# Kernel tuning notes

Measured on AMD Instinct MI355X. Metric: run time of the kernel, lower is better.

The kernel has to match this reference:

```python
import jax, jax.numpy as jnp
import numpy as np

B = 32          # patients
D = 128         # hidden dim (modality_embedding_dim == total_hidden_dim)
H = 4           # attention heads
DH = D // H     # per-head dim
L = 2           # num_graph_layers
N = {'ct': 1024, 'pet': 1024, 'clin': 256, 'gen': 2048, 'pat': 1}
# (src_type, dst_type) for the 8 relation types registered in _setup_relations
REL = [('ct','ct'), ('pet','pet'), ('clin','clin'), ('gen','gen'),
       ('pat','clin'), ('ct','gen'), ('pet','gen'), ('gen','pat')]
E_REL = [8192, 8192, 2048, 16384, 256, 8192, 8192, 2048]
EDGE_NAMES = ['e_ct','e_pet','e_clin','e_gen','e_pat2clin','e_ct2gen','e_pet2gen','e_gen2pat']


def setup_inputs() -> dict:
    key = jax.random.key(0)
    ks = iter(jax.random.split(key, 64))
    nk = lambda: next(ks)
    inp = {}
    inp['x_ct']   = jax.random.normal(nk(), (B, N['ct'],  D), jnp.float32)
    inp['x_pet']  = jax.random.normal(nk(), (B, N['pet'], D), jnp.float32)
    inp['x_clin'] = jax.random.normal(nk(), (B, N['clin'],D), jnp.float32)
    inp['x_gen']  = jax.random.normal(nk(), (B, N['gen'], D), jnp.float32)
    inp['early']  = jax.random.normal(nk(), (B, D), jnp.float32)

    def mk_edges(k, E, ns, nd):
        k1, k2 = jax.random.split(k)
        src = jax.random.randint(k1, (B, 1, E), 0, ns, jnp.int32)
        dst = jax.random.randint(k2, (B, 1, E), 0, nd, jnp.int32)
        return jnp.concatenate([src, dst], axis=1)  # [B,2,E]

    for nm, (s, d), E in zip(EDGE_NAMES, REL, E_REL):
        inp[nm] = mk_edges(nk(), E, N[s], N[d])

    sw = 1.0 / np.sqrt(D)
    inp['W_src'] = jax.random.normal(nk(), (L, 8, D, D), jnp.float32) * sw
    inp['W_dst'] = jax.random.normal(nk(), (L, 8, D, D), jnp.float32) * sw
    inp['a_src'] = jax.random.normal(nk(), (L, 8, H, DH), jnp.float32) * sw
    inp['a_dst'] = jax.random.normal(nk(), (L, 8, H, DH), jnp.float32) * sw
    inp['Wp'] = jax.random.normal(nk(), (3, D, D), jnp.float32) * sw  # CT, PET, genomic pooling
    inp['bp'] = jnp.zeros((3, D), jnp.float32)
    inp['W_sem'] = jax.random.normal(nk(), (4 * D, 128), jnp.float32) * (1.0 / np.sqrt(4 * D))
    inp['b_sem'] = jnp.zeros((128,), jnp.float32)
    inp['q_sem'] = jax.random.normal(nk(), (128,), jnp.float32) * sw
    return inp


def _leaky_relu(x):
    return jnp.where(x > 0, x, 0.2 * x)


def _gat_layer(x, edges, Ws, Wd, As, Ad):
    """One heterogeneous multi-head GAT layer summing over relation types."""
    agg = {t: jnp.zeros((B, N[t], H, DH), jnp.float32) for t in N}
    for r, ((s, d), ei) in enumerate(zip(REL, edges)):
        hs = jnp.einsum('bnd,de->bne', x[s], Ws[r]).reshape(B, N[s], H, DH)
        hd = jnp.einsum('bnd,de->bne', x[d], Wd[r]).reshape(B, N[d], H, DH)
        al_s = jnp.sum(hs * As[r], axis=-1)  # [B,Ns,H]
        al_d = jnp.sum(hd * Ad[r], axis=-1)  # [B,Nd,H]
        nd = N[d]

        def one(hs_b, as_b, ad_b, e_b):
            src, dst = e_b[0], e_b[1]
            logit = _leaky_relu(as_b[src] + ad_b[dst])                      # [E,H]
            m = jnp.full((nd, H), -1e30, logit.dtype).at[dst].max(logit)    # segment max
            p = jnp.exp(logit - m[dst])
            den = jnp.zeros((nd, H), p.dtype).at[dst].add(p)
            w = p / (den[dst] + 1e-16)                                      # edge softmax per dst node
            msg = w[:, :, None] * hs_b[src]                                 # [E,H,DH]
            return jnp.zeros((nd, H, DH), msg.dtype).at[dst].add(msg)

        agg[d] = agg[d] + jax.vmap(one)(hs, al_s, al_d, ei)
    return {t: jax.nn.elu(agg[t].reshape(B, N[t], D)) for t in N}


def _pool(feat, W, b):
    # query = Linear(mean(features)); scores = feat @ q; softmax-weighted sum
    q = jnp.mean(feat, axis=1) @ W + b            # [B,D]
    sc = jnp.einsum('bnd,bd->bn', feat, q)        # [B,N]
    w = jax.nn.softmax(sc, axis=1)
    return jnp.einsum('bn,bnd->bd', w, feat)      # [B,D]


def _forward(x_ct, x_pet, x_clin, x_gen, early, edges,
             W_src, W_dst, a_src, a_dst, Wp, bp, W_sem, b_sem, q_sem):
    x = {'ct': x_ct, 'pet': x_pet, 'clin': x_clin, 'gen': x_gen,
         'pat': early[:, None, :]}
    for l in range(L):
        x = _gat_layer(x, edges, W_src[l], W_dst[l], a_src[l], a_dst[l])
    ct_p  = _pool(x['ct'],  Wp[0], bp[0])
    pet_p = _pool(x['pet'], Wp[1], bp[1])
    gen_p = _pool(x['gen'], Wp[2], bp[2])   # shared across the 3 meta-paths
    pad = jnp.zeros((B, 2 * D), ct_p.dtype)  # pad 2D -> 4D as in original
    imm = jnp.concatenate([ct_p, gen_p, pad], axis=1)
    pro = jnp.concatenate([pet_p, gen_p, pad], axis=1)
    trt = jnp.concatenate([(ct_p + pet_p) * 0.5, gen_p, pad], axis=1)
    z = jnp.stack([imm, pro, trt], axis=1)                     # [B,3,4D]
    s = jnp.einsum('bpa,a->bp', jnp.tanh(jnp.einsum('bpf,fa->bpa', z, W_sem) + b_sem), q_sem)
    beta = jax.nn.softmax(s, axis=1)                           # [B,3]
    fused = jnp.einsum('bp,bpf->bf', beta, z)                  # [B,4D]
    return fused, beta


def reference(x_ct, x_pet, x_clin, x_gen, early,
              e_ct, e_pet, e_clin, e_gen, e_pat2clin, e_ct2gen, e_pet2gen, e_gen2pat,
              W_src, W_dst, a_src, a_dst, Wp, bp, W_sem, b_sem, q_sem):
    edges = [e_ct, e_pet, e_clin, e_gen, e_pat2clin, e_ct2gen, e_pet2gen, e_gen2pat]
    return _forward(x_ct, x_pet, x_clin, x_gen, early, edges,
                    W_src, W_dst, a_src, a_dst, Wp, bp, W_sem, b_sem, q_sem)
```

## Files before the change

kernel.cpp:

```cpp
#include <hip/hip_runtime.h>
#include <math.h>

static constexpr int NB = 32;
static constexpr int ND = 128;

typedef short bf16x8 __attribute__((ext_vector_type(8)));
typedef float f32x4  __attribute__((ext_vector_type(4)));
typedef unsigned short u16x8 __attribute__((ext_vector_type(8)));

__device__ __forceinline__ float lrelu(float x){ return x > 0.f ? x : 0.2f*x; }
__device__ __forceinline__ unsigned short f2b(float f){
  unsigned u = __float_as_uint(f);
  return (unsigned short)((u + 0x7FFFu + ((u>>16)&1u)) >> 16);
}
__device__ __forceinline__ float b2f(unsigned short b){
  return __uint_as_float(((unsigned)b) << 16);
}

__global__ __launch_bounds__(128) void k_fold(const float* __restrict__ Wsrc,
    const float* __restrict__ Wdst, const float* __restrict__ asrc,
    const float* __restrict__ adst, float* __restrict__ vbuf){
  const int wid[5] = {0,1,3,5,6};
  int lr = blockIdx.x, role = blockIdx.y, l = blockIdx.z;
  int r = wid[lr];
  const float* W = (role ? Wdst : Wsrc) + (size_t)(l*8+r)*16384;
  const float* a = (role ? adst : asrc) + (size_t)(l*8+r)*128;
  int k = threadIdx.x;
  float* o = vbuf + ((size_t)((l*5+lr)*2+role))*512 + k*4;
  #pragma unroll
  for(int h=0;h<4;h++){
    float s = 0.f;
    #pragma unroll
    for(int j=0;j<32;j++) s += W[k*128 + h*32 + j]*a[h*32 + j];
    o[h] = s;
  }
}

__global__ __launch_bounds__(256) void k_wpack(const float* __restrict__ Wsrc,
    unsigned short* __restrict__ Wf){
  const int wid[5] = {0,1,3,5,6};
  int lr = blockIdx.x, l = blockIdx.y;
  const float* W = Wsrc + (size_t)(l*8+wid[lr])*16384;
  unsigned short* o = Wf + (size_t)((l*5+lr)*4)*4096;
  for(int idx=threadIdx.x; idx<128*128; idx+=256){
    int k = idx >> 7, col = idx & 127;
    int h = col >> 5, cc = col & 31;
    int k4 = k>>2, g = k4&3, kk = k4>>3, j = 4*((k4>>2)&1) + (k&3);
    int nb = cc>>4, lane = (cc&15) + 16*g;
    o[(size_t)h*4096 + ((size_t)((kk*2+nb)*64 + lane))*8 + j] = f2b(W[k*128 + col]);
  }
}

__global__ __launch_bounds__(256) void k_conv(const float* __restrict__ i0,
    const float* __restrict__ i1, const float* __restrict__ i2,
    unsigned short* __restrict__ x16){
  int bx = blockIdx.x;
  const float* src; size_t base; unsigned short* dst;
  if(bx < 2048){ src=i0; base=(size_t)bx*2048; dst=x16; }
  else if(bx < 4096){ src=i1; base=(size_t)(bx-2048)*2048; dst=x16+4194304; }
  else { src=i2; base=(size_t)(bx-4096)*2048; dst=x16+8388608; }
  size_t o = base + (size_t)threadIdx.x*8;
  float4 a = *(const float4*)(src+o), b = *(const float4*)(src+o+4);
  u16x8 r;
  r[0]=f2b(a.x); r[1]=f2b(a.y); r[2]=f2b(a.z); r[3]=f2b(a.w);
  r[4]=f2b(b.x); r[5]=f2b(b.y); r[6]=f2b(b.z); r[7]=f2b(b.w);
  *(u16x8*)(dst+o) = r;
}

struct CsrP {
  const int* eg[5];
  int l2E[5];
  int Nd_[5];
  int roff_[5];
  int eoff_[5];
};

__global__ __launch_bounds__(512) void k_csr(CsrP P, int* __restrict__ rowstart,
                                             int* __restrict__ srcidx){
  int b = blockIdx.x, r = blockIdx.y, t = threadIdx.x;
  int E = 1<<P.l2E[r], Nd = P.Nd_[r];
  const int* eg = P.eg[r] + (size_t)b*2*E;
  int* rsO = rowstart + P.roff_[r] + b*(Nd+1);
  int* siO = srcidx + P.eoff_[r] + (size_t)b*E;
  __shared__ int cnt[2048];
  __shared__ int stmp[512];
  for(int i=t;i<Nd;i+=512) cnt[i]=0;
  __syncthreads();
  for(int e=t;e<E;e+=512) atomicAdd(&cnt[eg[E+e]], 1);
  __syncthreads();
  int carry=0;
  for(int c0=0;c0<Nd;c0+=512){
    int idx=c0+t;
    int v=(idx<Nd)?cnt[idx]:0;
    stmp[t]=v; __syncthreads();
    for(int off=1;off<512;off<<=1){
      int u=(t>=off)?stmp[t-off]:0;
      __syncthreads();
      stmp[t]+=u;
      __syncthreads();
    }
    int excl=stmp[t]-v+carry;
    if(idx<Nd){ rsO[idx]=excl; cnt[idx]=excl; }
    int tot = stmp[511];
    __syncthreads();
    carry+=tot;
  }
  if(t==0) rsO[Nd]=carry;
  __syncthreads();
  for(int e=t;e<E;e+=512){
    int src=eg[e], dst=eg[E+e];
    int pos=atomicAdd(&cnt[dst],1);
    siO[pos]=src;
  }
}

struct HsP {
  int tb[4];
  unsigned long long xoff[3];
  int Ns[3];
  int nW[3];
  unsigned long long wfo[3][2];
  unsigned long long hso[3][2];
  unsigned long long aso[3][2];
  unsigned long long asrco[3][2];
  int nvd[3];
  unsigned long long vdo[3][3];
  unsigned long long aldo2[3][3];
  int ndd[3][3];
};

__global__ __launch_bounds__(256) void k_hs(HsP P, const unsigned short* __restrict__ x16,
    const unsigned short* __restrict__ Wf, const float* __restrict__ asrc,
    const float* __restrict__ vbuf, unsigned short* __restrict__ hs,
    float* __restrict__ als, float* __restrict__ ald){
  __shared__ unsigned short xl[16*132];
  int B = blockIdx.x;
  int t=0; while(t<2 && B>=P.tb[t+1]) t++;
  int local = B - P.tb[t];
  int b = local & 31, tile = local >> 5;
  int n0 = tile*16;
  int tid = threadIdx.x, w = tid>>6, ln = tid&63;
  {
    int row = tid>>4, ch = tid&15;
    u16x8 v = *(const u16x8*)(x16 + P.xoff[t] + ((size_t)((size_t)b*P.Ns[t] + n0+row)*128 + ch*8));
    *(u16x8*)&xl[row*132 + ch*8] = v;
  }
  __syncthreads();
  int g = ln>>4, r15 = ln&15;
  for(int rep=0; rep<P.nW[t]; rep++){
    const unsigned short* wf = Wf + P.wfo[t][rep] + (size_t)w*4096;
    f32x4 acc[2]; acc[0]=(f32x4){0,0,0,0}; acc[1]=(f32x4){0,0,0,0};
    #pragma unroll
    for(int kk=0;kk<4;kk++){
      const unsigned short* pa = &xl[r15*132 + kk*32 + 4*g];
      ushort4 lo = *(const ushort4*)pa;
      ushort4 hi = *(const ushort4*)(pa+16);
      union { ushort u[8]; bf16x8 v; } tmp;
      tmp.u[0]=lo.x; tmp.u[1]=lo.y; tmp.u[2]=lo.z; tmp.u[3]=lo.w;
      tmp.u[4]=hi.x; tmp.u[5]=hi.y; tmp.u[6]=hi.z; tmp.u[7]=hi.w;
      bf16x8 af = tmp.v;
      #pragma unroll
      for(int nb=0;nb<2;nb++){
        bf16x8 bw = *(const bf16x8*)(wf + ((size_t)((kk*2+nb)*64 + ln))*8);
        acc[nb] = __builtin_amdgcn_mfma_f32_16x16x32_bf16(af, bw, acc[nb], 0, 0, 0);
      }
    }
    unsigned short* ho = hs + P.hso[t][rep] + ((size_t)b*P.Ns[t] + n0)*128;
    #pragma unroll
    for(int qq=0;qq<4;qq++){
      int m = 4*g + qq;
      #pragma unroll
      for(int nb=0;nb<2;nb++){
        ho[(size_t)m*128 + w*32 + nb*16 + r15] = f2b(acc[nb][qq]);
      }
    }
    {
      const float* aS = asrc + P.asrco[t][rep];
      float a0v = aS[w*32 + r15], a1v = aS[w*32 + 16 + r15];
      float p0 = acc[0][0]*a0v + acc[1][0]*a1v;
      float p1 = acc[0][1]*a0v + acc[1][1]*a1v;
      float p2 = acc[0][2]*a0v + acc[1][2]*a1v;
      float p3 = acc[0][3]*a0v + acc[1][3]*a1v;
      #pragma unroll
      for(int off=1; off<16; off<<=1){
        p0 += __shfl_xor(p0,off); p1 += __shfl_xor(p1,off);
        p2 += __shfl_xor(p2,off); p3 += __shfl_xor(p3,off);
      }
      if(r15 < 4){
        float pv = (r15==0)?p0:((r15==1)?p1:((r15==2)?p2:p3));
        als[P.aso[t][rep] + ((size_t)b*P.Ns[t] + n0 + 4*g + r15)*4 + w] = pv;
      }
    }
  }
  int nvd = P.nvd[t];
  if(tid < (nvd<<6)){
    int vd = tid>>6, rem = tid&63, row = rem>>2, h = rem&3;
    const float* vv = vbuf + P.vdo[t][vd];
    float s = 0.f;
    #pragma unroll 8
    for(int k=0;k<128;k++) s += b2f(xl[row*132+k]) * vv[k*4+h];
    ald[P.aldo2[t][vd] + ((size_t)b*P.ndd[t][vd] + n0 + row)*4 + h] = s;
  }
}

static constexpr int MAXE4 = 1536;
static constexpr int WST4  = 1544;

struct Fu4P {
  int tboff[4];
  int nrel[3], ndshift[3];
  int roff[3][3], eoff[3][3], E[3][3], Ns[3][3];
  unsigned long long aoff[3][3], aldo[3][3];
  unsigned long long hoff[3][3];
  unsigned long long outoff[3];
};

__global__ __launch_bounds__(512, 8) void k_fuse4(Fu4P P,
    const int* __restrict__ rowstart, const int* __restrict__ srcidx,
    const float* __restrict__ als, const float* __restrict__ ald,
    const unsigned short* __restrict__ hs, unsigned short* __restrict__ out16){
  __shared__ float wlds[4*WST4];
  __shared__ int   silds[MAXE4];
  __shared__ float aldl[3*256];
  __shared__ int   rsl[3*65];
  __shared__ int   ebo[3], baseo[3];
  int B = blockIdx.x;
  int t=0; while(t<2 && B>=P.tboff[t+1]) t++;
  int local = B - P.tboff[t];
  int b = local & 31, dtile = local >> 5;
  int Nd = 1 << P.ndshift[t];
  int d0 = dtile * 64;
  int tid = threadIdx.x, w = tid>>6, ln = tid&63;
  int nrel = P.nrel[t];

  {
    int acc_base = 0;
    #pragma unroll
    for(int q=0;q<3;q++){
      if(q < nrel){
        const int* rsq = rowstart + P.roff[t][q] + b*(Nd+1) + d0;
        int eb = rsq[0];
        int cnt = rsq[64] - eb;
        if(tid==0){ ebo[q]=eb; baseo[q]=acc_base; }
        for(int i=tid; i<65; i+=512) rsl[q*65+i] = rsq[i];
        const float* aldq = ald + P.aldo[t][q] + ((size_t)b*Nd + d0)*4;
        for(int i=tid; i<256; i+=512) aldl[(q<<8)+i] = aldq[i];
        const int* si = srcidx + P.eoff[t][q] + (size_t)b*P.E[t][q] + eb;
        for(int e=tid; e<cnt; e+=512) silds[acc_base + e] = si[e];
        acc_base += cnt;
      }
    }
  }
  __syncthreads();

  for(int s=tid; s<(nrel<<8); s+=512){
    int q = s>>8, rem = s&255, dloc = rem>>2, j = rem&3;
    int eb = ebo[q], bo = baseo[q];
    int e0 = bo + rsl[q*65+dloc] - eb;
    int e1 = bo + rsl[q*65+dloc+1] - eb;
    const float* alsb = als + P.aoff[t][q] + (size_t)b*P.Ns[t][q]*4;
    float4 ad4 = *(const float4*)&aldl[(q<<8) + (dloc<<2)];
    for(int e=e0+j; e<e1; e+=4){
      int sidx = silds[e];
      float4 as4 = *(const float4*)(alsb + (size_t)sidx*4);
      wlds[0*WST4+e] = lrelu(as4.x+ad4.x);
      wlds[1*WST4+e] = lrelu(as4.y+ad4.y);
      wlds[2*WST4+e] = lrelu(as4.z+ad4.z);
      wlds[3*WST4+e] = lrelu(as4.w+ad4.w);
    }
  }
  __syncthreads();

  for(int s=tid; s<(nrel<<8); s+=512){
    int q = s>>8, rem = s&255, dloc = rem>>2, h2 = rem&3;
    int eb = ebo[q], bo = baseo[q];
    int e0 = bo + rsl[q*65+dloc] - eb;
    int e1 = bo + rsl[q*65+dloc+1] - eb;
    float* wrow = &wlds[h2*WST4];
    float m = -1e30f;
    for(int e=e0;e<e1;e++) m = fmaxf(m, wrow[e]);
    float den = 0.f;
    for(int e=e0;e<e1;e++){ float p=__expf(wrow[e]-m); wrow[e]=p; den+=p; }
    float inv = 1.f/(den + 1e-16f);
    for(int e=e0;e<e1;e++) wrow[e] *= inv;
  }
  __syncthreads();

  int h = ln>>4;
  float accA[8], accB[8];
  #pragma unroll
  for(int i=0;i<8;i++){ accA[i]=0.f; accB[i]=0.f; }
  for(int q=0;q<nrel;q++){
    const unsigned short* hb = hs + P.hoff[t][q] + (size_t)b*P.Ns[t][q]*128;
    int eb = ebo[q], bo = baseo[q];
    #pragma unroll
    for(int it=0; it<8; it++){
      int dloc = w*8 + it;
      int e0 = bo + rsl[q*65+dloc] - eb;
      int e1 = bo + rsl[q*65+dloc+1] - eb;
      float a0 = 0.f, a1 = 0.f;
      int e = e0;
      int eal = (e0+3)&~3; if(eal > e1) eal = e1;
      for(; e<eal; e++){
        float wv = wlds[h*WST4 + e];
        unsigned v = *(const unsigned*)(hb + ((size_t)silds[e]*128 + 2*ln));
        a0 += wv*__uint_as_float(v<<16);
        a1 += wv*__uint_as_float(v&0xFFFF0000u);
      }
      for(; e+4<=e1; e+=4){
        int4  sq = *(const int4*)&silds[e];
        float4 wq = *(const float4*)&wlds[h*WST4 + e];
        unsigned v0 = *(const unsigned*)(hb + ((size_t)sq.x*128 + 2*ln));
        unsigned v1 = *(const unsigned*)(hb + ((size_t)sq.y*128 + 2*ln));
        unsigned v2 = *(const unsigned*)(hb + ((size_t)sq.z*128 + 2*ln));
        unsigned v3 = *(const unsigned*)(hb + ((size_t)sq.w*128 + 2*ln));
        a0 += wq.x*__uint_as_float(v0<<16); a1 += wq.x*__uint_as_float(v0&0xFFFF0000u);
        a0 += wq.y*__uint_as_float(v1<<16); a1 += wq.y*__uint_as_float(v1&0xFFFF0000u);
        a0 += wq.z*__uint_as_float(v2<<16); a1 += wq.z*__uint_as_float(v2&0xFFFF0000u);
        a0 += wq.w*__uint_as_float(v3<<16); a1 += wq.w*__uint_as_float(v3&0xFFFF0000u);
      }
      for(; e<e1; e++){
        float wv = wlds[h*WST4 + e];
        unsigned v = *(const unsigned*)(hb + ((size_t)silds[e]*128 + 2*ln));
        a0 += wv*__uint_as_float(v<<16);
        a1 += wv*__uint_as_float(v&0xFFFF0000u);
      }
      accA[it] += a0; accB[it] += a1;
    }
  }
  #pragma unroll
  for(int it=0; it<8; it++){
    int m = d0 + w*8 + it;
    float v0 = accA[it], v1 = accB[it];
    v0 = v0 > 0.f ? v0 : expm1f(v0);
    v1 = v1 > 0.f ? v1 : expm1f(v1);
    ushort2 o; o.x = f2b(v0); o.y = f2b(v1);
    *(ushort2*)(out16 + P.outoff[t] + ((size_t)b*Nd + m)*128 + 2*ln) = o;
  }
}

__device__ __constant__ const size_t POFF[3] = {0ull, 4194304ull, 8388608ull};
__device__ __constant__ const int    PNN[3]  = {1024, 1024, 2048};
static constexpr int PCH = 64;
static constexpr int MAXCH = 32;

__global__ __launch_bounds__(128) void k_pool_psum(const unsigned short* __restrict__ x2,
    float* __restrict__ part){
  int p = blockIdx.z, b = blockIdx.x, c = blockIdx.y, t = threadIdx.x;
  int Nn = PNN[p];
  if(c*PCH >= Nn) return;
  const unsigned short* f = x2 + POFF[p] + ((size_t)b*Nn + c*PCH)*ND;
  float acc = 0.f;
  #pragma unroll 8
  for(int n=0;n<PCH;n++) acc += b2f(f[(size_t)n*ND + t]);
  part[(((size_t)p*NB + b)*MAXCH + c)*ND + t] = acc;
}

__global__ __launch_bounds__(128) void k_pool_q(const float* __restrict__ part,
    const float* __restrict__ Wp, const float* __restrict__ bp,
    float* __restrict__ q){
  int p = blockIdx.z, b = blockIdx.x, t = threadIdx.x;
  int nch = PNN[p]/PCH;
  __shared__ float mean[ND];
  float s = 0.f;
  for(int c=0;c<nch;c++) s += part[(((size_t)p*NB + b)*MAXCH + c)*ND + t];
  mean[t] = s / (float)PNN[p];
  __syncthreads();
  const float* W = Wp + (size_t)p*ND*ND;
  float qv = bp[p*ND + t];
  #pragma unroll 8
  for(int k=0;k<ND;k++) qv += mean[k]*W[k*ND + t];
  q[((size_t)p*NB + b)*ND + t] = qv;
}

__global__ __launch_bounds__(256) void k_pool_score(const unsigned short* __restrict__ x2,
    const float* __restrict__ q, float* __restrict__ sc){
  int p = blockIdx.z, b = blockIdx.y;
  int w = threadIdx.x >> 6, lane = threadIdx.x & 63;
  int n = blockIdx.x*4 + w;
  int Nn = PNN[p];
  if(n >= Nn) return;
  const unsigned short* f  = x2 + POFF[p] + ((size_t)b*Nn + n)*ND;
  const float* qb = q + ((size_t)p*NB + b)*ND;
  float s = b2f(f[lane])*qb[lane] + b2f(f[lane+64])*qb[lane+64];
  #pragma unroll
  for(int off=32; off; off>>=1) s += __shfl_xor(s, off);
  if(lane == 0) sc[((size_t)p*NB + b)*2048 + n] = s;
}

__global__ __launch_bounds__(256) void k_pool_smax(const float* __restrict__ sc,
    float* __restrict__ stat){
  int p = blockIdx.z, b = blockIdx.x, t = threadIdx.x;
  int Nn = PNN[p];
  __shared__ float red[256];
  const float* s = sc + ((size_t)p*NB + b)*2048;
  float mx = -1e30f;
  for(int n=t;n<Nn;n+=256) mx = fmaxf(mx, s[n]);
  red[t] = mx; __syncthreads();
  for(int o=128;o;o>>=1){ if(t<o) red[t]=fmaxf(red[t],red[t+o]); __syncthreads(); }
  mx = red[0]; __syncthreads();
  float sum = 0.f;
  for(int n=t;n<Nn;n+=256) sum += __expf(s[n]-mx);
  red[t] = sum; __syncthreads();
  for(int o=128;o;o>>=1){ if(t<o) red[t]+=red[t+o]; __syncthreads(); }
  if(t==0){ stat[((size_t)p*NB + b)*2] = mx; stat[((size_t)p*NB + b)*2+1] = 1.f/red[0]; }
}

__global__ __launch_bounds__(128) void k_pool_wsum(const unsigned short* __restrict__ x2,
    const float* __restrict__ sc, const float* __restrict__ stat,
    float* __restrict__ part){
  int p = blockIdx.z, b = blockIdx.x, c = blockIdx.y, t = threadIdx.x;
  int Nn = PNN[p];
  if(c*PCH >= Nn) return;
  __shared__ float wsh[PCH];
  float mx  = stat[((size_t)p*NB + b)*2];
  float inv = stat[((size_t)p*NB + b)*2+1];
  if(t < PCH) wsh[t] = __expf(sc[((size_t)p*NB + b)*2048 + c*PCH + t] - mx)*inv;
  __syncthreads();
  const unsigned short* f = x2 + POFF[p] + ((size_t)b*Nn + c*PCH)*ND;
  float acc = 0.f;
  #pragma unroll 8
  for(int n=0;n<PCH;n++) acc += wsh[n]*b2f(f[(size_t)n*ND + t]);
  part[(((size_t)p*NB + b)*MAXCH + c)*ND + t] = acc;
}

__global__ __launch_bounds__(128) void k_pool_comb(const float* __restrict__ part,
    float* __restrict__ pooled){
  int p = blockIdx.z, b = blockIdx.x, t = threadIdx.x;
  int nch = PNN[p]/PCH;
  float s = 0.f;
  for(int c=0;c<nch;c++) s += part[(((size_t)p*NB + b)*MAXCH + c)*ND + t];
  pooled[((size_t)p*NB + b)*ND + t] = s;
}

__global__ __launch_bounds__(128) void k_sem(const float* __restrict__ ctp,
    const float* __restrict__ petp, const float* __restrict__ genp,
    const float* __restrict__ Wsem, const float* __restrict__ bsem,
    const float* __restrict__ qsem, float* __restrict__ fused, float* __restrict__ beta){
  int b = blockIdx.x, t = threadIdx.x;
  __shared__ float z[3][256];
  __shared__ float red[128];
  float ct = ctp[b*ND + t], pet = petp[b*ND + t], gen = genp[b*ND + t];
  z[0][t]=ct;  z[1][t]=pet; z[2][t]=0.5f*(ct+pet);
  z[0][ND+t]=gen; z[1][ND+t]=gen; z[2][ND+t]=gen;
  __syncthreads();
  float s[3];
  for(int p=0;p<3;p++){
    float a = bsem[t];
    for(int f=0;f<256;f++) a += z[p][f]*Wsem[f*128 + t];
    a = tanhf(a);
    red[t] = a * qsem[t];
    __syncthreads();
    for(int o=64;o>0;o>>=1){ if(t<o) red[t]+=red[t+o]; __syncthreads(); }
    s[p] = red[0]; __syncthreads();
  }
  float mx = fmaxf(s[0], fmaxf(s[1], s[2]));
  float e0 = __expf(s[0]-mx), e1 = __expf(s[1]-mx), e2 = __expf(s[2]-mx);
  float sm = e0+e1+e2;
  float b0 = e0/sm, b1 = e1/sm, b2 = e2/sm;
  if(t < 3) beta[b*3 + t] = (t==0)?b0:((t==1)?b1:b2);
  float f0 = b0*z[0][t] + b1*z[1][t] + b2*z[2][t];
  float f1 = b0*z[0][ND+t] + b1*z[1][ND+t] + b2*z[2][ND+t];
  fused[(size_t)b*512 + t]       = f0;
  fused[(size_t)b*512 + 128 + t] = f1;
  fused[(size_t)b*512 + 256 + t] = 0.f;
  fused[(size_t)b*512 + 384 + t] = 0.f;
}

extern "C" void kernel_launch(void* const* d_in, const int* in_sizes, int n_in,
                              void* d_out, int out_size, void* d_ws, size_t ws_size,
                              hipStream_t stream) {
  static const int wid[5]    = {0,1,3,5,6};
  static const int edgein[5] = {5,6,8,10,11};
  static const int l2E[5]    = {13,13,14,13,13};
  static const int Nd_l[5]   = {1024,1024,2048,2048,2048};
  static const int E_l[5]    = {8192,8192,16384,8192,8192};
  static const int Ns_l[5]   = {1024,1024,2048,1024,1024};
  static const int eoff[6]   = {0,262144,524288,1048576,1310720,1572864};
  static const int roff[5]   = {0,32800,65600,131168,196736};
  static const unsigned long long aoff[5]   = {0,131072,262144,524288,655360};
  static const unsigned long long aldoff[5] = {0,131072,262144,524288,786432};
  static const unsigned long long hsoff_lr[5] = {0ull,4194304ull,8388608ull,16777216ull,20971520ull};
  static const unsigned long long ALD = 786432;

  const float* Wsrc = (const float*)d_in[13];
  const float* Wp   = (const float*)d_in[17];
  const float* bp   = (const float*)d_in[18];
  const float* Wsem = (const float*)d_in[19];
  const float* bsem = (const float*)d_in[20];
  const float* qsem = (const float*)d_in[21];

  unsigned short* xc16 = (unsigned short*)d_ws;
  unsigned short* x2b16 = xc16;
  unsigned short* xmid16 = xc16 + 16777216;
  float* albase = (float*)(xmid16 + 16777216);
  float* als = albase;
  float* ald = albase + ALD;
  float* vbuf = albase + 1835008;
  unsigned short* wfbuf = (unsigned short*)(vbuf + 10240);
  float* pooled = (float*)(wfbuf + 163840);
  float* part = pooled + 12288;
  float* qbuf = part + 393216;
  float* scbuf = qbuf + 12288;
  float* stat = scbuf + 196608;
  int* rowstart = (int*)(stat + 192);
  int* srcidx = rowstart + 262304;
  unsigned short* hs16 = (unsigned short*)(srcidx + 1572864);

  { dim3 g(5,2,2); k_fold<<<g,128,0,stream>>>(Wsrc, (const float*)d_in[14],
                                              (const float*)d_in[15], (const float*)d_in[16], vbuf); }
  { dim3 g(5,2); k_wpack<<<g,256,0,stream>>>(Wsrc, wfbuf); }

  CsrP csr;
  for(int r=0;r<5;r++){
    csr.eg[r] = (const int*)d_in[edgein[r]];
    csr.l2E[r] = l2E[r]; csr.Nd_[r] = Nd_l[r];
    csr.roff_[r] = roff[r]; csr.eoff_[r] = eoff[r];
  }
  { dim3 g(NB,5); k_csr<<<g,512,0,stream>>>(csr, rowstart, srcidx); }

  k_conv<<<8192,256,0,stream>>>((const float*)d_in[0], (const float*)d_in[1],
                                (const float*)d_in[3], xc16);

  static const unsigned long long xoo[3] = {0,4194304,8388608};
  static const int t2_nrel[3] = {3,1,1};
  static const int t2_lrel[3][3] = {{2,3,4},{0,0,0},{1,0,0}};
  static const int t2_nds[3] = {11,10,10};
  static const int t2_out[3] = {2,0,1};

  Fu4P fp;
  fp.tboff[0]=0; fp.tboff[1]=1024; fp.tboff[2]=1536; fp.tboff[3]=2048;
  for(int t=0;t<3;t++){
    fp.nrel[t]=t2_nrel[t]; fp.ndshift[t]=t2_nds[t]; fp.outoff[t]=xoo[t2_out[t]];
    for(int q=0;q<3;q++){
      int lr = t2_lrel[t][q];
      fp.roff[t][q]=roff[lr]; fp.eoff[t][q]=eoff[lr];
      fp.E[t][q]=E_l[lr]; fp.Ns[t][q]=Ns_l[lr];
      fp.aoff[t][q]=aoff[lr]; fp.aldo[t][q]=aldoff[lr];
      fp.hoff[t][q]=hsoff_lr[lr];
    }
  }

  static const int hs_lr[3][2] = {{0,3},{1,4},{2,2}};
  static const int vd_lr[3][3] = {{0,0,0},{1,0,0},{2,3,4}};
  HsP hp;
  hp.tb[0]=0; hp.tb[1]=2048; hp.tb[2]=4096; hp.tb[3]=8192;
  hp.xoff[0]=0; hp.xoff[1]=4194304; hp.xoff[2]=8388608;
  hp.Ns[0]=1024; hp.Ns[1]=1024; hp.Ns[2]=2048;
  hp.nW[0]=2; hp.nW[1]=2; hp.nW[2]=1;
  hp.nvd[0]=1; hp.nvd[1]=1; hp.nvd[2]=3;
  for(int t=0;t<3;t++){
    for(int rep=0;rep<2;rep++){
      int lr = hs_lr[t][rep];
      hp.hso[t][rep]=hsoff_lr[lr];
      hp.aso[t][rep]=aoff[lr];
    }
    for(int vd=0;vd<3;vd++){
      int lr = vd_lr[t][vd];
      hp.aldo2[t][vd]=aldoff[lr];
      hp.ndd[t][vd]=Nd_l[lr];
    }
  }
  hp.hso[2][1]=0; hp.aso[2][1]=0;

  for(int l=0;l<2;l++){
    const unsigned short* xcur = (l==0) ? xc16 : xmid16;
    unsigned short* xout = (l==0) ? xmid16 : x2b16;

    for(int t=0;t<3;t++){
      for(int rep=0;rep<2;rep++){
        int lr = hs_lr[t][rep];
        hp.wfo[t][rep]=(unsigned long long)((l*5 + lr)*4)*4096;
        hp.asrco[t][rep]=(unsigned long long)((l*8 + wid[lr])*128);
      }
      for(int vd=0;vd<3;vd++){
        int lr = vd_lr[t][vd];
        hp.vdo[t][vd]=((unsigned long long)((l*5+lr)*2+1))*512;
      }
    }
    k_hs<<<8192,256,0,stream>>>(hp, xcur, wfbuf, (const float*)d_in[15], vbuf,
                                hs16, als, ald);

    k_fuse4<<<2048,512,0,stream>>>(fp, rowstart, srcidx, als, ald, hs16, xout);
  }

  {
    dim3 gchunk(NB, MAXCH, 3);
    dim3 gone(NB, 1, 3);
    dim3 gscore(512, NB, 3);
    k_pool_psum <<<gchunk,128,0,stream>>>(x2b16, part);
    k_pool_q    <<<gone,  128,0,stream>>>(part, Wp, bp, qbuf);
    k_pool_score<<<gscore,256,0,stream>>>(x2b16, qbuf, scbuf);
    k_pool_smax <<<gone,  256,0,stream>>>(scbuf, stat);
    k_pool_wsum <<<gchunk,128,0,stream>>>(x2b16, scbuf, stat, part);
    k_pool_comb <<<gone,  128,0,stream>>>(part, pooled);
  }

  float* fused = (float*)d_out;
  float* beta  = fused + (size_t)NB*512;
  k_sem<<<NB,128,0,stream>>>(pooled, pooled + NB*ND, pooled + 2*NB*ND,
                             Wsem, bsem, qsem, fused, beta);
}
```

Before: 366.7 us.

## Fuse fp32→bf16 conversion into k_hs and restructure fused GAT aggregation

Drops the separate k_conv pass. In layer 0, k_hs now reads the fp32 inputs directly and converts them to bf16 in its shared-memory tile load. The aggregation kernel is reworked: edges from all relations are merged per destination row into one CSR in LDS, with source indices pre-offset to global rows, and a single loop runs over relations unrolled by 8. Blocks are remapped so each XCD handles a fixed set of patients, which should help L2 locality. The extra prefix-sum and index-baking passes add synchronisation and integer work.

```diff
diff --git a/kernel.cpp b/kernel.cpp
--- a/kernel.cpp
+++ b/kernel.cpp
@@ -51,22 +51,6 @@
   }
 }
 
-__global__ __launch_bounds__(256) void k_conv(const float* __restrict__ i0,
-    const float* __restrict__ i1, const float* __restrict__ i2,
-    unsigned short* __restrict__ x16){
-  int bx = blockIdx.x;
-  const float* src; size_t base; unsigned short* dst;
-  if(bx < 2048){ src=i0; base=(size_t)bx*2048; dst=x16; }
-  else if(bx < 4096){ src=i1; base=(size_t)(bx-2048)*2048; dst=x16+4194304; }
-  else { src=i2; base=(size_t)(bx-4096)*2048; dst=x16+8388608; }
-  size_t o = base + (size_t)threadIdx.x*8;
-  float4 a = *(const float4*)(src+o), b = *(const float4*)(src+o+4);
-  u16x8 r;
-  r[0]=f2b(a.x); r[1]=f2b(a.y); r[2]=f2b(a.z); r[3]=f2b(a.w);
-  r[4]=f2b(b.x); r[5]=f2b(b.y); r[6]=f2b(b.z); r[7]=f2b(b.w);
-  *(u16x8*)(dst+o) = r;
-}
-
 struct CsrP {
   const int* eg[5];
   int l2E[5];
@@ -116,6 +100,8 @@
 
 struct HsP {
   int tb[4];
+  int usef;
+  const float* xf[3];
   unsigned long long xoff[3];
   int Ns[3];
   int nW[3];
@@ -140,7 +126,16 @@
   int b = local & 31, tile = local >> 5;
   int n0 = tile*16;
   int tid = threadIdx.x, w = tid>>6, ln = tid&63;
-  {
+  if(P.usef){
+    const float* xf = P.xf[t] + ((size_t)((size_t)b*P.Ns[t] + n0))*128;
+    int row = tid>>4, c8 = tid&15;
+    float4 a = *(const float4*)(xf + (size_t)row*128 + c8*8);
+    float4 c = *(const float4*)(xf + (size_t)row*128 + c8*8 + 4);
+    u16x8 r;
+    r[0]=f2b(a.x); r[1]=f2b(a.y); r[2]=f2b(a.z); r[3]=f2b(a.w);
+    r[4]=f2b(c.x); r[5]=f2b(c.y); r[6]=f2b(c.z); r[7]=f2b(c.w);
+    *(u16x8*)&xl[row*132 + c8*8] = r;
+  } else {
     int row = tid>>4, ch = tid&15;
     u16x8 v = *(const u16x8*)(x16 + P.xoff[t] + ((size_t)((size_t)b*P.Ns[t] + n0+row)*128 + ch*8));
     *(u16x8*)&xl[row*132 + ch*8] = v;
@@ -204,18 +199,17 @@
 }
 
 static constexpr int MAXE4 = 1536;
-static constexpr int WST4  = 1544;
-
-struct Fu4P {
-  int tboff[4];
+static constexpr int WST4  = 1548;
+
+struct Fu5P {
   int nrel[3], ndshift[3];
   int roff[3][3], eoff[3][3], E[3][3], Ns[3][3];
-  unsigned long long aoff[3][3], aldo[3][3];
-  unsigned long long hoff[3][3];
+  int rowbase[3][3];
+  unsigned long long aldo[3][3];
   unsigned long long outoff[3];
 };
 
-__global__ __launch_bounds__(512, 8) void k_fuse4(Fu4P P,
+__global__ __launch_bounds__(512, 8) void k_fuse5(Fu5P P,
     const int* __restrict__ rowstart, const int* __restrict__ srcidx,
     const float* __restrict__ als, const float* __restrict__ ald,
     const unsigned short* __restrict__ hs, unsigned short* __restrict__ out16){
@@ -223,46 +217,59 @@
   __shared__ int   silds[MAXE4];
   __shared__ float aldl[3*256];
   __shared__ int   rsl[3*65];
-  __shared__ int   ebo[3], baseo[3];
+  __shared__ int   crs[65];
+  __shared__ int   cst[3*64];
   int B = blockIdx.x;
-  int t=0; while(t<2 && B>=P.tboff[t+1]) t++;
-  int local = B - P.tboff[t];
-  int b = local & 31, dtile = local >> 5;
+  int xcd = B & 7, slot = B >> 3;
+  int bg = slot >> 6, rem = slot & 63;
+  int b = bg*8 + xcd;
+  int t, dtile;
+  if(rem < 32){ t = 0; dtile = rem; }
+  else if(rem < 48){ t = 1; dtile = rem - 32; }
+  else { t = 2; dtile = rem - 48; }
   int Nd = 1 << P.ndshift[t];
   int d0 = dtile * 64;
   int tid = threadIdx.x, w = tid>>6, ln = tid&63;
   int nrel = P.nrel[t];
 
-  {
-    int acc_base = 0;
-    #pragma unroll
-    for(int q=0;q<3;q++){
-      if(q < nrel){
-        const int* rsq = rowstart + P.roff[t][q] + b*(Nd+1) + d0;
-        int eb = rsq[0];
-        int cnt = rsq[64] - eb;
-        if(tid==0){ ebo[q]=eb; baseo[q]=acc_base; }
-        for(int i=tid; i<65; i+=512) rsl[q*65+i] = rsq[i];
-        const float* aldq = ald + P.aldo[t][q] + ((size_t)b*Nd + d0)*4;
-        for(int i=tid; i<256; i+=512) aldl[(q<<8)+i] = aldq[i];
-        const int* si = srcidx + P.eoff[t][q] + (size_t)b*P.E[t][q] + eb;
-        for(int e=tid; e<cnt; e+=512) silds[acc_base + e] = si[e];
-        acc_base += cnt;
-      }
-    }
-  }
-  __syncthreads();
-
+  for(int q=0;q<nrel;q++){
+    const int* rsq = rowstart + P.roff[t][q] + b*(Nd+1) + d0;
+    for(int i=tid;i<65;i+=512) rsl[q*65+i] = rsq[i];
+    const float* aldq = ald + P.aldo[t][q] + ((size_t)b*Nd + d0)*4;
+    for(int i=tid;i<256;i+=512) aldl[(q<<8)+i] = aldq[i];
+  }
+  __syncthreads();
+  if(tid < 65){
+    int s = 0;
+    for(int q=0;q<nrel;q++) s += rsl[q*65+tid] - rsl[q*65];
+    crs[tid] = s;
+  } else if(tid >= 128 && tid < 128 + nrel*64){
+    int q = (tid-128)>>6, d = (tid-128)&63;
+    int s = 0;
+    for(int q2=0;q2<nrel;q2++) s += rsl[q2*65+d] - rsl[q2*65];
+    for(int q2=0;q2<q;q2++)    s += rsl[q2*65+d+1] - rsl[q2*65+d];
+    cst[q*64+d] = s;
+  }
+  __syncthreads();
   for(int s=tid; s<(nrel<<8); s+=512){
-    int q = s>>8, rem = s&255, dloc = rem>>2, j = rem&3;
-    int eb = ebo[q], bo = baseo[q];
-    int e0 = bo + rsl[q*65+dloc] - eb;
-    int e1 = bo + rsl[q*65+dloc+1] - eb;
-    const float* alsb = als + P.aoff[t][q] + (size_t)b*P.Ns[t][q]*4;
-    float4 ad4 = *(const float4*)&aldl[(q<<8) + (dloc<<2)];
-    for(int e=e0+j; e<e1; e+=4){
-      int sidx = silds[e];
-      float4 as4 = *(const float4*)(alsb + (size_t)sidx*4);
+    int q = s>>8, r2 = s&255, dloc = r2>>2, j = r2&3;
+    const int* si = srcidx + P.eoff[t][q] + (size_t)b*P.E[t][q];
+    int rs0 = rsl[q*65+dloc];
+    int deg = rsl[q*65+dloc+1] - rs0;
+    int cb = cst[q*64+dloc];
+    int bake = P.rowbase[t][q] + b*P.Ns[t][q];
+    for(int i=j;i<deg;i+=4) silds[cb+i] = bake + si[rs0+i];
+  }
+  __syncthreads();
+  for(int s=tid; s<(nrel<<8); s+=512){
+    int q = s>>8, r2 = s&255, dloc = r2>>2, j = r2&3;
+    int deg = rsl[q*65+dloc+1] - rsl[q*65+dloc];
+    int cb = cst[q*64+dloc];
+    float4 ad4 = *(const float4*)&aldl[(q<<8)+(dloc<<2)];
+    for(int i=j;i<deg;i+=4){
+      int e = cb+i;
+      int sil = silds[e];
+      float4 as4 = *(const float4*)(als + 4*(size_t)sil);
       wlds[0*WST4+e] = lrelu(as4.x+ad4.x);
       wlds[1*WST4+e] = lrelu(as4.y+ad4.y);
       wlds[2*WST4+e] = lrelu(as4.z+ad4.z);
@@ -270,12 +277,10 @@
     }
   }
   __syncthreads();
-
   for(int s=tid; s<(nrel<<8); s+=512){
-    int q = s>>8, rem = s&255, dloc = rem>>2, h2 = rem&3;
-    int eb = ebo[q], bo = baseo[q];
-    int e0 = bo + rsl[q*65+dloc] - eb;
-    int e1 = bo + rsl[q*65+dloc+1] - eb;
+    int q = s>>8, r2 = s&255, dloc = r2>>2, h2 = r2&3;
+    int e0 = cst[q*64+dloc];
+    int e1 = e0 + rsl[q*65+dloc+1] - rsl[q*65+dloc];
     float* wrow = &wlds[h2*WST4];
     float m = -1e30f;
     for(int e=e0;e<e1;e++) m = fmaxf(m, wrow[e]);
@@ -285,48 +290,64 @@
     for(int e=e0;e<e1;e++) wrow[e] *= inv;
   }
   __syncthreads();
-
   int h = ln>>4;
   float accA[8], accB[8];
   #pragma unroll
   for(int i=0;i<8;i++){ accA[i]=0.f; accB[i]=0.f; }
-  for(int q=0;q<nrel;q++){
-    const unsigned short* hb = hs + P.hoff[t][q] + (size_t)b*P.Ns[t][q]*128;
-    int eb = ebo[q], bo = baseo[q];
-    #pragma unroll
-    for(int it=0; it<8; it++){
-      int dloc = w*8 + it;
-      int e0 = bo + rsl[q*65+dloc] - eb;
-      int e1 = bo + rsl[q*65+dloc+1] - eb;
-      float a0 = 0.f, a1 = 0.f;
-      int e = e0;
-      int eal = (e0+3)&~3; if(eal > e1) eal = e1;
-      for(; e<eal; e++){
-        float wv = wlds[h*WST4 + e];
-        unsigned v = *(const unsigned*)(hb + ((size_t)silds[e]*128 + 2*ln));
-        a0 += wv*__uint_as_float(v<<16);
-        a1 += wv*__uint_as_float(v&0xFFFF0000u);
-      }
-      for(; e+4<=e1; e+=4){
-        int4  sq = *(const int4*)&silds[e];
-        float4 wq = *(const float4*)&wlds[h*WST4 + e];
-        unsigned v0 = *(const unsigned*)(hb + ((size_t)sq.x*128 + 2*ln));
-        unsigned v1 = *(const unsigned*)(hb + ((size_t)sq.y*128 + 2*ln));
-        unsigned v2 = *(const unsigned*)(hb + ((size_t)sq.z*128 + 2*ln));
-        unsigned v3 = *(const unsigned*)(hb + ((size_t)sq.w*128 + 2*ln));
-        a0 += wq.x*__uint_as_float(v0<<16); a1 += wq.x*__uint_as_float(v0&0xFFFF0000u);
-        a0 += wq.y*__uint_as_float(v1<<16); a1 += wq.y*__uint_as_float(v1&0xFFFF0000u);
-        a0 += wq.z*__uint_as_float(v2<<16); a1 += wq.z*__uint_as_float(v2&0xFFFF0000u);
-        a0 += wq.w*__uint_as_float(v3<<16); a1 += wq.w*__uint_as_float(v3&0xFFFF0000u);
-      }
-      for(; e<e1; e++){
-        float wv = wlds[h*WST4 + e];
-        unsigned v = *(const unsigned*)(hb + ((size_t)silds[e]*128 + 2*ln));
-        a0 += wv*__uint_as_float(v<<16);
-        a1 += wv*__uint_as_float(v&0xFFFF0000u);
-      }
-      accA[it] += a0; accB[it] += a1;
-    }
+  #pragma unroll
+  for(int it=0; it<8; it++){
+    int dloc = w*8 + it;
+    int e0 = crs[dloc], e1 = crs[dloc+1];
+    float a0 = 0.f, a1 = 0.f;
+    int e = e0;
+    int eal = (e0+3)&~3; if(eal > e1) eal = e1;
+    for(; e<eal; e++){
+      float wv = wlds[h*WST4 + e];
+      unsigned v = *(const unsigned*)(hs + ((size_t)silds[e]*128 + 2*ln));
+      a0 += wv*__uint_as_float(v<<16);
+      a1 += wv*__uint_as_float(v&0xFFFF0000u);
+    }
+    for(; e+8<=e1; e+=8){
+      int4  sq0 = *(const int4*)&silds[e];
+      int4  sq1 = *(const int4*)&silds[e+4];
+      float4 wq0 = *(const float4*)&wlds[h*WST4 + e];
+      float4 wq1 = *(const float4*)&wlds[h*WST4 + e + 4];
+      unsigned v0 = *(const unsigned*)(hs + ((size_t)sq0.x*128 + 2*ln));
+      unsigned v1 = *(const unsigned*)(hs + ((size_t)sq0.y*128 + 2*ln));
+      unsigned v2 = *(const unsigned*)(hs + ((size_t)sq0.z*128 + 2*ln));
+      unsigned v3 = *(const unsigned*)(hs + ((size_t)sq0.w*128 + 2*ln));
+      unsigned v4 = *(const unsigned*)(hs + ((size_t)sq1.x*128 + 2*ln));
+      unsigned v5 = *(const unsigned*)(hs + ((size_t)sq1.y*128 + 2*ln));
+      unsigned v6 = *(const unsigned*)(hs + ((size_t)sq1.z*128 + 2*ln));
+      unsigned v7 = *(const unsigned*)(hs + ((size_t)sq1.w*128 + 2*ln));
+      a0 += wq0.x*__uint_as_float(v0<<16); a1 += wq0.x*__uint_as_float(v0&0xFFFF0000u);
+      a0 += wq0.y*__uint_as_float(v1<<16); a1 += wq0.y*__uint_as_float(v1&0xFFFF0000u);
+      a0 += wq0.z*__uint_as_float(v2<<16); a1 += wq0.z*__uint_as_float(v2&0xFFFF0000u);
+      a0 += wq0.w*__uint_as_float(v3<<16); a1 += wq0.w*__uint_as_float(v3&0xFFFF0000u);
+      a0 += wq1.x*__uint_as_float(v4<<16); a1 += wq1.x*__uint_as_float(v4&0xFFFF0000u);
+      a0 += wq1.y*__uint_as_float(v5<<16); a1 += wq1.y*__uint_as_float(v5&0xFFFF0000u);
+      a0 += wq1.z*__uint_as_float(v6<<16); a1 += wq1.z*__uint_as_float(v6&0xFFFF0000u);
+      a0 += wq1.w*__uint_as_float(v7<<16); a1 += wq1.w*__uint_as_float(v7&0xFFFF0000u);
+    }
+    for(; e+4<=e1; e+=4){
+      int4  sq = *(const int4*)&silds[e];
+      float4 wq = *(const float4*)&wlds[h*WST4 + e];
+      unsigned v0 = *(const unsigned*)(hs + ((size_t)sq.x*128 + 2*ln));
+      unsigned v1 = *(const unsigned*)(hs + ((size_t)sq.y*128 + 2*ln));
+      unsigned v2 = *(const unsigned*)(hs + ((size_t)sq.z*128 + 2*ln));
+      unsigned v3 = *(const unsigned*)(hs + ((size_t)sq.w*128 + 2*ln));
+      a0 += wq.x*__uint_as_float(v0<<16); a1 += wq.x*__uint_as_float(v0&0xFFFF0000u);
+      a0 += wq.y*__uint_as_float(v1<<16); a1 += wq.y*__uint_as_float(v1&0xFFFF0000u);
+      a0 += wq.z*__uint_as_float(v2<<16); a1 += wq.z*__uint_as_float(v2&0xFFFF0000u);
+      a0 += wq.w*__uint_as_float(v3<<16); a1 += wq.w*__uint_as_float(v3&0xFFFF0000u);
+    }
+    for(; e<e1; e++){
+      float wv = wlds[h*WST4 + e];
+      unsigned v = *(const unsigned*)(hs + ((size_t)silds[e]*128 + 2*ln));
+      a0 += wv*__uint_as_float(v<<16);
+      a1 += wv*__uint_as_float(v&0xFFFF0000u);
+    }
+    accA[it] = a0; accB[it] = a1;
   }
   #pragma unroll
   for(int it=0; it<8; it++){
@@ -519,25 +540,21 @@
   }
   { dim3 g(NB,5); k_csr<<<g,512,0,stream>>>(csr, rowstart, srcidx); }
 
-  k_conv<<<8192,256,0,stream>>>((const float*)d_in[0], (const float*)d_in[1],
-                                (const float*)d_in[3], xc16);
-
   static const unsigned long long xoo[3] = {0,4194304,8388608};
   static const int t2_nrel[3] = {3,1,1};
   static const int t2_lrel[3][3] = {{2,3,4},{0,0,0},{1,0,0}};
   static const int t2_nds[3] = {11,10,10};
   static const int t2_out[3] = {2,0,1};
 
-  Fu4P fp;
-  fp.tboff[0]=0; fp.tboff[1]=1024; fp.tboff[2]=1536; fp.tboff[3]=2048;
+  Fu5P fp;
   for(int t=0;t<3;t++){
     fp.nrel[t]=t2_nrel[t]; fp.ndshift[t]=t2_nds[t]; fp.outoff[t]=xoo[t2_out[t]];
     for(int q=0;q<3;q++){
       int lr = t2_lrel[t][q];
       fp.roff[t][q]=roff[lr]; fp.eoff[t][q]=eoff[lr];
       fp.E[t][q]=E_l[lr]; fp.Ns[t][q]=Ns_l[lr];
-      fp.aoff[t][q]=aoff[lr]; fp.aldo[t][q]=aldoff[lr];
-      fp.hoff[t][q]=hsoff_lr[lr];
+      fp.rowbase[t][q]=(int)(aoff[lr]/4);
+      fp.aldo[t][q]=aldoff[lr];
     }
   }
 
@@ -545,6 +562,7 @@
   static const int vd_lr[3][3] = {{0,0,0},{1,0,0},{2,3,4}};
   HsP hp;
   hp.tb[0]=0; hp.tb[1]=2048; hp.tb[2]=4096; hp.tb[3]=8192;
+  hp.xf[0]=(const float*)d_in[0]; hp.xf[1]=(const float*)d_in[1]; hp.xf[2]=(const float*)d_in[3];
   hp.xoff[0]=0; hp.xoff[1]=4194304; hp.xoff[2]=8388608;
   hp.Ns[0]=1024; hp.Ns[1]=1024; hp.Ns[2]=2048;
   hp.nW[0]=2; hp.nW[1]=2; hp.nW[2]=1;
@@ -564,8 +582,8 @@
   hp.hso[2][1]=0; hp.aso[2][1]=0;
 
   for(int l=0;l<2;l++){
-    const unsigned short* xcur = (l==0) ? xc16 : xmid16;
     unsigned short* xout = (l==0) ? xmid16 : x2b16;
+    hp.usef = (l==0) ? 1 : 0;
 
     for(int t=0;t<3;t++){
       for(int rep=0;rep<2;rep++){
@@ -578,10 +596,10 @@
         hp.vdo[t][vd]=((unsigned long long)((l*5+lr)*2+1))*512;
       }
     }
-    k_hs<<<8192,256,0,stream>>>(hp, xcur, wfbuf, (const float*)d_in[15], vbuf,
+    k_hs<<<8192,256,0,stream>>>(hp, xmid16, wfbuf, (const float*)d_in[15], vbuf,
                                 hs16, als, ald);
 
-    k_fuse4<<<2048,512,0,stream>>>(fp, rowstart, srcidx, als, ald, hs16, xout);
+    k_fuse5<<<2048,512,0,stream>>>(fp, rowstart, srcidx, als, ald, hs16, xout);
   }
 
   {
```

Result: faster. 336.0 us (-8.4%).
